# Optimization experiments

Hardware: AMD Instinct MI355X
Metric: run time of the kernel (lower is better)

Reference implementation:

```python
import jax, jax.numpy as jnp
import numpy as np

N_NODES = 100000
N_EDGES = 800000
VOCAB = 100
D_FEAT = 10
D = 64
EPS = 1e-8  # torch F.cosine_similarity eps


def setup_inputs() -> dict:
    key = jax.random.key(0)
    ks = jax.random.split(key, 8)
    return {
        "nodes": jax.random.randint(ks[0], (N_NODES,), 0, VOCAB),
        "edges": jax.random.randint(ks[1], (N_EDGES, 2), 0, N_NODES),
        "features": jax.random.normal(ks[2], (N_NODES, D_FEAT), dtype=jnp.float32),
        "node_emb": jax.random.normal(ks[3], (VOCAB, D), dtype=jnp.float32),
        "feat_W": jax.random.normal(ks[4], (D, D_FEAT), dtype=jnp.float32) * 0.1,
        "feat_b": jnp.zeros((D,), dtype=jnp.float32),
        "conv1_W": jax.random.normal(ks[5], (D, D), dtype=jnp.float32) * 0.1,
        "conv1_b": jnp.zeros((D,), dtype=jnp.float32),
        "pattern_emb": jax.random.normal(ks[6], (VOCAB, D), dtype=jnp.float32),
        "pattern_id": 42,  # hash(node_type) % 100
    }


def reference(nodes, edges, features, node_emb, feat_W, feat_b,
              conv1_W, conv1_b, pattern_emb, pattern_id):
    # initial embeddings: type embedding + linear feature projection  [N, D]
    embeds = node_emb[nodes] + (features @ feat_W.T + feat_b)

    src, dst = edges[:, 0], edges[:, 1]
    for _ in range(2):  # fixed 2 message-passing rounds (structural loop)
        # scatter-add messages from src to dst (order-independent sum)
        agg = jnp.zeros_like(embeds).at[dst].add(embeds[src])
        embeds = jax.nn.relu((embeds + agg) @ conv1_W.T + conv1_b)

    # cosine similarity of each node embedding against the pattern embedding
    p = pattern_emb[pattern_id]  # [D]
    num = embeds @ p  # [N]
    denom = jnp.maximum(jnp.linalg.norm(embeds, axis=1), EPS) * \
            jnp.maximum(jnp.linalg.norm(p), EPS)
    return num / denom  # [N] match scores
```

## Files before the change

kernel.cpp:

```cpp
#include <hip/hip_runtime.h>
#include <hip/hip_bf16.h>

#define N_NODES 100000
#define N_EDGES 800000
#define D 64
#define SCAN_B 256
#define NB1 ((N_NODES + SCAN_B - 1) / SCAN_B)
#define FILL_BLOCKS (N_EDGES / 256)
#define INIT_BLOCKS (N_NODES * D / 256)
#define CT 64
#define XS 68
#define OS 72

__device__ __forceinline__ unsigned short f2bf(float f) {
    union { float f; unsigned u; } v; v.f = f;
    unsigned r = v.u + 0x7fffu + ((v.u >> 16) & 1u);
    return (unsigned short)(r >> 16);
}
__device__ __forceinline__ float bf2f(unsigned short u) {
    return __uint_as_float(((unsigned)u) << 16);
}
__device__ __forceinline__ void acc_bf8(float acc[8], uint4 u) {
    acc[0] += __uint_as_float(u.x << 16);
    acc[1] += __uint_as_float(u.x & 0xffff0000u);
    acc[2] += __uint_as_float(u.y << 16);
    acc[3] += __uint_as_float(u.y & 0xffff0000u);
    acc[4] += __uint_as_float(u.z << 16);
    acc[5] += __uint_as_float(u.z & 0xffff0000u);
    acc[6] += __uint_as_float(u.w << 16);
    acc[7] += __uint_as_float(u.w & 0xffff0000u);
}

__global__ __launch_bounds__(256) void hist_rank_kernel(
        const int2* __restrict__ edges,
        int* __restrict__ deg,
        int* __restrict__ rank) {
    int t = blockIdx.x * 256 + threadIdx.x;
    int2 e = edges[t];
    rank[t] = atomicAdd(&deg[e.y], 1);
}

__global__ void scan1_kernel(const int* __restrict__ deg,
                             int* __restrict__ row_ptr,
                             int* __restrict__ bsum) {
    __shared__ int tmp[SCAN_B];
    int t = threadIdx.x;
    int i = blockIdx.x * SCAN_B + t;
    int v = (i < N_NODES) ? deg[i] : 0;
    tmp[t] = v;
    __syncthreads();
#pragma unroll
    for (int off = 1; off < SCAN_B; off <<= 1) {
        int a = (t >= off) ? tmp[t - off] : 0;
        __syncthreads();
        tmp[t] += a;
        __syncthreads();
    }
    if (i < N_NODES) row_ptr[i] = tmp[t] - v;
    if (t == SCAN_B - 1) bsum[blockIdx.x] = tmp[t];
}

__global__ void scan23_kernel(int* __restrict__ row_ptr,
                              const int* __restrict__ bsum) {
    __shared__ int red[SCAN_B];
    int t = threadIdx.x;
    int partial = 0;
    if (t < blockIdx.x && t < NB1) partial += bsum[t];
    int t2 = t + 256;
    if (t2 < blockIdx.x && t2 < NB1) partial += bsum[t2];
    red[t] = partial;
    __syncthreads();
#pragma unroll
    for (int off = 128; off > 0; off >>= 1) {
        if (t < off) red[t] += red[t + off];
        __syncthreads();
    }
    int boff = red[0];
    int i = blockIdx.x * SCAN_B + t;
    if (i < N_NODES) row_ptr[i] += boff;
    if (i == 0) row_ptr[N_NODES] = N_EDGES;
}

__global__ __launch_bounds__(256) void fill_init_kernel(
        const int2* __restrict__ edges,
        const int* __restrict__ rank,
        const int* __restrict__ rowp,
        int* __restrict__ col,
        const int* __restrict__ nodes,
        const float* __restrict__ features,
        const float* __restrict__ node_emb,
        const float* __restrict__ feat_W,
        const float* __restrict__ feat_b,
        unsigned short* __restrict__ embeds) {
    if (blockIdx.x < FILL_BLOCKS) {
        int t = blockIdx.x * 256 + threadIdx.x;
        int2 e = edges[t];
        col[rowp[e.y] + rank[t]] = e.x;
    } else {
        int tid = (blockIdx.x - FILL_BLOCKS) * 256 + threadIdx.x;
        int node = tid >> 6;
        int d = tid & 63;
        float acc = feat_b[d];
        const float* f = features + (size_t)node * 10;
        const float* w = feat_W + (size_t)d * 10;
#pragma unroll
        for (int j = 0; j < 10; ++j) acc += f[j] * w[j];
        embeds[tid] = f2bf(node_emb[(size_t)nodes[node] * D + d] + acc);
    }
}

template <bool SCORE>
__global__ __launch_bounds__(512, 8) void gconv_kernel(
        const unsigned short* __restrict__ emb_in,
        const int* __restrict__ rowp,
        const int* __restrict__ col,
        const float* __restrict__ W,
        const float* __restrict__ b,
        const float* __restrict__ pattern_emb,
        const int* __restrict__ pattern_id,
        unsigned short* __restrict__ emb_out,
        float* __restrict__ score_out) {
    __shared__ float Xs[CT][XS];
    __shared__ union {
        float W4[CT][XS];
        unsigned short Os[CT][OS];
    } u;
    __shared__ float ps[D];

    int t = threadIdx.x;
    int base = blockIdx.x * CT;
    int lane = t & 63;
    int wv = t >> 6;

    {
        int c = t & 15;
        int r = t >> 4;
#pragma unroll
        for (int p = 0; p < 2; ++p) {
            int rr = r + 32 * p;
            *((float4*)&u.W4[rr][4 * c]) = ((const float4*)(W + (size_t)rr * D))[c];
        }
    }
    if (SCORE && t < D) ps[t] = pattern_emb[(size_t)pattern_id[0] * D + t];

    int g = lane >> 3;
    int c8 = lane & 7;
    int rp = 0;
    if (lane <= 8) {
        int nidx = base + wv * 8 + lane;
        rp = rowp[nidx <= N_NODES ? nidx : N_NODES];
    }

    for (int nn = 0; nn < 8; ++nn) {
        int rl = wv * 8 + nn;
        int node = base + rl;
        int start = __shfl(rp, nn, 64);
        int end   = __shfl(rp, nn + 1, 64);

        float acc[8];
#pragma unroll
        for (int j = 0; j < 8; ++j) acc[j] = 0.f;
        if (g == 0 && node < N_NODES) {
            uint4 uu = ((const uint4*)(emb_in + (size_t)node * D))[c8];
            acc_bf8(acc, uu);
        }

        for (int b2 = start; b2 < end; b2 += 32) {
            int nb = end - b2; if (nb > 32) nb = 32;
            int idx = (lane < nb) ? col[b2 + lane] : 0;
#pragma unroll
            for (int r = 0; r < 4; ++r) {
                int s = r * 8 + g;
                int src = __shfl(idx, s, 64);
                if (s < nb) {
                    uint4 uu = ((const uint4*)(emb_in + (size_t)src * D))[c8];
                    acc_bf8(acc, uu);
                }
            }
        }

#pragma unroll
        for (int m = 8; m <= 32; m <<= 1)
#pragma unroll
            for (int j = 0; j < 8; ++j) acc[j] += __shfl_xor(acc[j], m, 64);

        if (g == 0) {
            *((float4*)&Xs[rl][8 * c8])     = make_float4(acc[0], acc[1], acc[2], acc[3]);
            *((float4*)&Xs[rl][8 * c8 + 4]) = make_float4(acc[4], acc[5], acc[6], acc[7]);
        }
    }
    __syncthreads();

    int i = t & 15;
    int j = t >> 4;
    float bj0 = b[j], bj1 = b[j + 32];

    float acc2[4][2] = {};
    for (int k4 = 0; k4 < 16; ++k4) {
        float4 xr[4], wr[2];
#pragma unroll
        for (int di = 0; di < 4; ++di) xr[di] = *((const float4*)&Xs[i + 16 * di][4 * k4]);
        wr[0] = *((const float4*)&u.W4[j][4 * k4]);
        wr[1] = *((const float4*)&u.W4[j + 32][4 * k4]);
#pragma unroll
        for (int di = 0; di < 4; ++di)
#pragma unroll
            for (int dj = 0; dj < 2; ++dj)
                acc2[di][dj] += xr[di].x * wr[dj].x + xr[di].y * wr[dj].y
                              + xr[di].z * wr[dj].z + xr[di].w * wr[dj].w;
    }

    if (!SCORE) {
        __syncthreads();
#pragma unroll
        for (int di = 0; di < 4; ++di) {
            u.Os[i + 16 * di][j]      = f2bf(fmaxf(acc2[di][0] + bj0, 0.f));
            u.Os[i + 16 * di][j + 32] = f2bf(fmaxf(acc2[di][1] + bj1, 0.f));
        }
        __syncthreads();
        int r = t >> 3, seg = t & 7;
        int node = base + r;
        if (node < N_NODES)
            ((uint4*)(emb_out + (size_t)node * D))[seg] = *((const uint4*)&u.Os[r][8 * seg]);
    } else {
        __syncthreads();
#pragma unroll
        for (int di = 0; di < 4; ++di) {
            Xs[i + 16 * di][j]      = fmaxf(acc2[di][0] + bj0, 0.f);
            Xs[i + 16 * di][j + 32] = fmaxf(acc2[di][1] + bj1, 0.f);
        }
        __syncthreads();
        if (t < CT) {
            float dot = 0.f, n2 = 0.f, pn = 0.f;
#pragma unroll 8
            for (int k = 0; k < D; ++k) {
                float yk = Xs[t][k];
                float pk = ps[k];
                dot += yk * pk; n2 += yk * yk; pn += pk * pk;
            }
            int node = base + t;
            if (node < N_NODES)
                score_out[node] = dot / (fmaxf(sqrtf(n2), 1e-8f) * fmaxf(sqrtf(pn), 1e-8f));
        }
    }
}

__global__ void init_embeds_kernel(const int* __restrict__ nodes,
                                   const float* __restrict__ features,
                                   const float* __restrict__ node_emb,
                                   const float* __restrict__ feat_W,
                                   const float* __restrict__ feat_b,
                                   float* __restrict__ embeds) {
    int tid = blockIdx.x * blockDim.x + threadIdx.x;
    if (tid >= N_NODES * D) return;
    int node = tid >> 6;
    int d = tid & 63;
    float acc = feat_b[d];
    const float* f = features + (size_t)node * 10;
    const float* w = feat_W + (size_t)d * 10;
#pragma unroll
    for (int j = 0; j < 10; ++j) acc += f[j] * w[j];
    embeds[tid] = node_emb[(size_t)nodes[node] * D + d] + acc;
}

__global__ void scatter_add_kernel(const int* __restrict__ edges,
                                   const float* __restrict__ embeds,
                                   float* __restrict__ agg) {
    int tid = blockIdx.x * blockDim.x + threadIdx.x;
    int edge = tid >> 6;
    int lane = tid & 63;
    if (edge >= N_EDGES) return;
    int src = edges[2 * edge + 0];
    int dst = edges[2 * edge + 1];
    atomicAdd(&agg[(size_t)dst * D + lane], embeds[(size_t)src * D + lane]);
}

__global__ void conv_inplace_kernel(const float* __restrict__ agg,
                                    const float* __restrict__ W,
                                    const float* __restrict__ b,
                                    float* __restrict__ embeds) {
    __shared__ float Ws[D * 65];
    __shared__ float xs[4][D];
    for (int i = threadIdx.x; i < D * D; i += blockDim.x) {
        int d = i >> 6, k = i & 63;
        Ws[d * 65 + k] = W[i];
    }
    __syncthreads();
    int lane_d = threadIdx.x & 63;
    int local_n = threadIdx.x >> 6;
    float bias = b[lane_d];
    const int n_chunks = (N_NODES + 3) / 4;
    for (int chunk = blockIdx.x; chunk < n_chunks; chunk += gridDim.x) {
        int node = chunk * 4 + local_n;
        if (node < N_NODES) {
            size_t base = (size_t)node * D + lane_d;
            xs[local_n][lane_d] = embeds[base] + agg[base];
        }
        __syncthreads();
        if (node < N_NODES) {
            float acc = bias;
#pragma unroll
            for (int k = 0; k < D; ++k) acc += xs[local_n][k] * Ws[lane_d * 65 + k];
            embeds[(size_t)node * D + lane_d] = fmaxf(acc, 0.0f);
        }
        __syncthreads();
    }
}

__global__ void final_score_kernel(const float* __restrict__ embeds,
                                   const float* __restrict__ pattern_emb,
                                   const int* __restrict__ pattern_id,
                                   float* __restrict__ out) {
    int lane = threadIdx.x & 63;
    int wave = threadIdx.x >> 6;
    int node = blockIdx.x * 4 + wave;
    int pid = pattern_id[0];
    float p = pattern_emb[(size_t)pid * D + lane];
    float pn = p * p;
#pragma unroll
    for (int m = 32; m > 0; m >>= 1) pn += __shfl_xor(pn, m, 64);
    if (node < N_NODES) {
        float e = embeds[(size_t)node * D + lane];
        float dot = e * p;
        float n2 = e * e;
#pragma unroll
        for (int m = 32; m > 0; m >>= 1) {
            dot += __shfl_xor(dot, m, 64);
            n2  += __shfl_xor(n2, m, 64);
        }
        if (lane == 0) {
            float denom = fmaxf(sqrtf(n2), 1e-8f) * fmaxf(sqrtf(pn), 1e-8f);
            out[node] = dot / denom;
        }
    }
}

extern "C" void kernel_launch(void* const* d_in, const int* in_sizes, int n_in,
                              void* d_out, int out_size, void* d_ws, size_t ws_size,
                              hipStream_t stream) {
    const int*   nodes       = (const int*)d_in[0];
    const int*   edges       = (const int*)d_in[1];
    const float* features    = (const float*)d_in[2];
    const float* node_emb    = (const float*)d_in[3];
    const float* feat_W      = (const float*)d_in[4];
    const float* feat_b      = (const float*)d_in[5];
    const float* conv1_W     = (const float*)d_in[6];
    const float* conv1_b     = (const float*)d_in[7];
    const float* pattern_emb = (const float*)d_in[8];
    const int*   pattern_id  = (const int*)d_in[9];
    float* out = (float*)d_out;

    const size_t emb_f32_bytes = (size_t)N_NODES * D * sizeof(float);
    const size_t emb_bf_bytes  = (size_t)N_NODES * D * 2;
    auto align256 = [](size_t x) { return (x + 255) & ~(size_t)255; };

    size_t o_embA = 0;
    size_t o_embB = o_embA + align256(emb_bf_bytes);
    size_t o_col  = o_embB + align256(emb_bf_bytes);
    size_t o_rank = o_col  + align256((size_t)N_EDGES * 4);
    size_t o_row  = o_rank + align256((size_t)N_EDGES * 4);
    size_t o_deg  = o_row  + align256((size_t)(N_NODES + 1) * 4);
    size_t o_bsum = o_deg  + align256((size_t)N_NODES * 4);
    size_t need   = o_bsum + align256((size_t)NB1 * 4);

    char* ws = (char*)d_ws;

    if (ws_size >= need) {
        unsigned short* embA = (unsigned short*)(ws + o_embA);
        unsigned short* embB = (unsigned short*)(ws + o_embB);
        int*   col  = (int*)(ws + o_col);
        int*   rank = (int*)(ws + o_rank);
        int*   rowp = (int*)(ws + o_row);
        int*   deg  = (int*)(ws + o_deg);
        int*   bsum = (int*)(ws + o_bsum);

        hipMemsetAsync(deg, 0, (size_t)N_NODES * 4, stream);
        hist_rank_kernel<<<FILL_BLOCKS, 256, 0, stream>>>((const int2*)edges, deg, rank);
        scan1_kernel<<<NB1, SCAN_B, 0, stream>>>(deg, rowp, bsum);
        scan23_kernel<<<NB1, SCAN_B, 0, stream>>>(rowp, bsum);
        fill_init_kernel<<<FILL_BLOCKS + INIT_BLOCKS, 256, 0, stream>>>(
            (const int2*)edges, rank, rowp, col,
            nodes, features, node_emb, feat_W, feat_b, embA);

        const int conv_grid = (N_NODES + CT - 1) / CT;

        gconv_kernel<false><<<conv_grid, 512, 0, stream>>>(
            embA, rowp, col, conv1_W, conv1_b, pattern_emb, pattern_id, embB, nullptr);
        gconv_kernel<true><<<conv_grid, 512, 0, stream>>>(
            embB, rowp, col, conv1_W, conv1_b, pattern_emb, pattern_id, nullptr, out);
    } else {
        float* embeds = (float*)ws;
        float* agg = (float*)(ws + align256(emb_f32_bytes));
        init_embeds_kernel<<<(N_NODES * D + 255) / 256, 256, 0, stream>>>(
            nodes, features, node_emb, feat_W, feat_b, embeds);
        for (int it = 0; it < 2; ++it) {
            hipMemsetAsync(agg, 0, emb_f32_bytes, stream);
            long long total = (long long)N_EDGES * 64;
            scatter_add_kernel<<<(int)((total + 255) / 256), 256, 0, stream>>>(edges, embeds, agg);
            conv_inplace_kernel<<<2048, 256, 0, stream>>>(agg, conv1_W, conv1_b, embeds);
        }
        final_score_kernel<<<(N_NODES + 3) / 4, 256, 0, stream>>>(
            embeds, pattern_emb, pattern_id, out);
    }
}
```

Measured before the change: 278.0 us.

## Restructure graph conv to one node per wavefront with in-register matvec

The conv kernel now assigns one node per 64-lane wavefront (4 nodes per 256-thread block) instead of 64 nodes per 512-thread block. The dense 64x64 transform is done per node in registers from a swizzled shared-memory copy of W, with a shuffle reduction, instead of a block-wide tiled GEMM. This removes the block-level syncs and the staging tiles in the epilogue, and the cosine score is computed with wave shuffles. In exchange every block reloads the full 16KB W into shared memory for only four nodes, and there are more shuffles per node.

Measured after the change: 332.4 us. 1.2x slower.

```diff
diff --git a/kernel.cpp b/kernel.cpp
--- a/kernel.cpp
+++ b/kernel.cpp
@@ -8,9 +8,6 @@
 #define NB1 ((N_NODES + SCAN_B - 1) / SCAN_B)
 #define FILL_BLOCKS (N_EDGES / 256)
 #define INIT_BLOCKS (N_NODES * D / 256)
-#define CT 64
-#define XS 68
-#define OS 72
 
 __device__ __forceinline__ unsigned short f2bf(float f) {
     union { float f; unsigned u; } v; v.f = f;
@@ -29,6 +26,9 @@
     acc[5] += __uint_as_float(u.z & 0xffff0000u);
     acc[6] += __uint_as_float(u.w << 16);
     acc[7] += __uint_as_float(u.w & 0xffff0000u);
+}
+__device__ __forceinline__ unsigned pack2bf(float a, float b) {
+    return (unsigned)f2bf(a) | ((unsigned)f2bf(b) << 16);
 }
 
 __global__ __launch_bounds__(256) void hist_rank_kernel(
@@ -110,7 +110,7 @@
 }
 
 template <bool SCORE>
-__global__ __launch_bounds__(512, 8) void gconv_kernel(
+__global__ __launch_bounds__(256, 6) void gatherconv_kernel(
         const unsigned short* __restrict__ emb_in,
         const int* __restrict__ rowp,
         const int* __restrict__ col,
@@ -120,128 +120,103 @@
         const int* __restrict__ pattern_id,
         unsigned short* __restrict__ emb_out,
         float* __restrict__ score_out) {
-    __shared__ float Xs[CT][XS];
-    __shared__ union {
-        float W4[CT][XS];
-        unsigned short Os[CT][OS];
-    } u;
-    __shared__ float ps[D];
+    __shared__ float Wl[4096];
+    __shared__ float bl[64];
+    __shared__ float ps[64];
 
     int t = threadIdx.x;
-    int base = blockIdx.x * CT;
+
+#pragma unroll
+    for (int q = 0; q < 4; ++q) {
+        int v = t + 256 * q;
+        float4 w4 = ((const float4*)W)[v];
+        int d  = v >> 4;
+        int k4 = v & 15;
+        int c  = k4 >> 1;
+        int i0 = (k4 & 1) * 4;
+        int slot = ((d & 7) * 64) + ((d >> 3) * 8) + c;
+        *((float4*)&Wl[slot * 8 + i0]) = w4;
+    }
+    if (t < 64) bl[t] = b[t];
+    if (SCORE && t < 64) ps[t] = pattern_emb[(size_t)pattern_id[0] * D + t];
+    __syncthreads();
+
     int lane = t & 63;
-    int wv = t >> 6;
-
-    {
-        int c = t & 15;
-        int r = t >> 4;
-#pragma unroll
-        for (int p = 0; p < 2; ++p) {
-            int rr = r + 32 * p;
-            *((float4*)&u.W4[rr][4 * c]) = ((const float4*)(W + (size_t)rr * D))[c];
-        }
-    }
-    if (SCORE && t < D) ps[t] = pattern_emb[(size_t)pattern_id[0] * D + t];
-
+    int wv   = t >> 6;
+    int node = blockIdx.x * 4 + wv;
     int g = lane >> 3;
-    int c8 = lane & 7;
-    int rp = 0;
-    if (lane <= 8) {
-        int nidx = base + wv * 8 + lane;
-        rp = rowp[nidx <= N_NODES ? nidx : N_NODES];
-    }
-
-    for (int nn = 0; nn < 8; ++nn) {
-        int rl = wv * 8 + nn;
-        int node = base + rl;
-        int start = __shfl(rp, nn, 64);
-        int end   = __shfl(rp, nn + 1, 64);
-
-        float acc[8];
-#pragma unroll
-        for (int j = 0; j < 8; ++j) acc[j] = 0.f;
-        if (g == 0 && node < N_NODES) {
-            uint4 uu = ((const uint4*)(emb_in + (size_t)node * D))[c8];
-            acc_bf8(acc, uu);
-        }
-
-        for (int b2 = start; b2 < end; b2 += 32) {
-            int nb = end - b2; if (nb > 32) nb = 32;
-            int idx = (lane < nb) ? col[b2 + lane] : 0;
-#pragma unroll
-            for (int r = 0; r < 4; ++r) {
-                int s = r * 8 + g;
-                int src = __shfl(idx, s, 64);
-                if (s < nb) {
-                    uint4 uu = ((const uint4*)(emb_in + (size_t)src * D))[c8];
-                    acc_bf8(acc, uu);
-                }
+    int c = lane & 7;
+
+    int start = rowp[node];
+    int end   = rowp[node + 1];
+
+    float acc[8];
+#pragma unroll
+    for (int j = 0; j < 8; ++j) acc[j] = 0.f;
+    if (g == 0) {
+        uint4 u = ((const uint4*)(emb_in + (size_t)node * D))[c];
+        acc_bf8(acc, u);
+    }
+
+    for (int base = start; base < end; base += 32) {
+        int nb = end - base; if (nb > 32) nb = 32;
+        int idx = (lane < nb) ? col[base + lane] : 0;
+#pragma unroll
+        for (int r = 0; r < 4; ++r) {
+            int s = r * 8 + g;
+            int src = __shfl(idx, s, 64);
+            if (s < nb) {
+                uint4 u = ((const uint4*)(emb_in + (size_t)src * D))[c];
+                acc_bf8(acc, u);
             }
         }
-
-#pragma unroll
-        for (int m = 8; m <= 32; m <<= 1)
-#pragma unroll
-            for (int j = 0; j < 8; ++j) acc[j] += __shfl_xor(acc[j], m, 64);
-
-        if (g == 0) {
-            *((float4*)&Xs[rl][8 * c8])     = make_float4(acc[0], acc[1], acc[2], acc[3]);
-            *((float4*)&Xs[rl][8 * c8 + 4]) = make_float4(acc[4], acc[5], acc[6], acc[7]);
-        }
-    }
-    __syncthreads();
-
-    int i = t & 15;
-    int j = t >> 4;
-    float bj0 = b[j], bj1 = b[j + 32];
-
-    float acc2[4][2] = {};
-    for (int k4 = 0; k4 < 16; ++k4) {
-        float4 xr[4], wr[2];
-#pragma unroll
-        for (int di = 0; di < 4; ++di) xr[di] = *((const float4*)&Xs[i + 16 * di][4 * k4]);
-        wr[0] = *((const float4*)&u.W4[j][4 * k4]);
-        wr[1] = *((const float4*)&u.W4[j + 32][4 * k4]);
-#pragma unroll
-        for (int di = 0; di < 4; ++di)
-#pragma unroll
-            for (int dj = 0; dj < 2; ++dj)
-                acc2[di][dj] += xr[di].x * wr[dj].x + xr[di].y * wr[dj].y
-                              + xr[di].z * wr[dj].z + xr[di].w * wr[dj].w;
-    }
+    }
+#pragma unroll
+    for (int m = 8; m <= 32; m <<= 1) {
+#pragma unroll
+        for (int j = 0; j < 8; ++j) acc[j] += __shfl_xor(acc[j], m, 64);
+    }
+
+    float y[8];
+#pragma unroll
+    for (int j = 0; j < 8; ++j) {
+        const float4* wp = (const float4*)&Wl[(j * 64 + lane) * 8];
+        float4 w0 = wp[0], w1 = wp[1];
+        y[j] = acc[0] * w0.x + acc[1] * w0.y + acc[2] * w0.z + acc[3] * w0.w
+             + acc[4] * w1.x + acc[5] * w1.y + acc[6] * w1.z + acc[7] * w1.w;
+    }
+#pragma unroll
+    for (int m = 1; m <= 4; m <<= 1) {
+#pragma unroll
+        for (int j = 0; j < 8; ++j) y[j] += __shfl_xor(y[j], m, 64);
+    }
+#pragma unroll
+    for (int j = 0; j < 8; ++j) y[j] = fmaxf(y[j] + bl[g * 8 + j], 0.f);
 
     if (!SCORE) {
-        __syncthreads();
-#pragma unroll
-        for (int di = 0; di < 4; ++di) {
-            u.Os[i + 16 * di][j]      = f2bf(fmaxf(acc2[di][0] + bj0, 0.f));
-            u.Os[i + 16 * di][j + 32] = f2bf(fmaxf(acc2[di][1] + bj1, 0.f));
-        }
-        __syncthreads();
-        int r = t >> 3, seg = t & 7;
-        int node = base + r;
-        if (node < N_NODES)
-            ((uint4*)(emb_out + (size_t)node * D))[seg] = *((const uint4*)&u.Os[r][8 * seg]);
+        if (c == 0) {
+            uint4 p;
+            p.x = pack2bf(y[0], y[1]);
+            p.y = pack2bf(y[2], y[3]);
+            p.z = pack2bf(y[4], y[5]);
+            p.w = pack2bf(y[6], y[7]);
+            ((uint4*)(emb_out + (size_t)node * D))[g] = p;
+        }
     } else {
-        __syncthreads();
-#pragma unroll
-        for (int di = 0; di < 4; ++di) {
-            Xs[i + 16 * di][j]      = fmaxf(acc2[di][0] + bj0, 0.f);
-            Xs[i + 16 * di][j + 32] = fmaxf(acc2[di][1] + bj1, 0.f);
-        }
-        __syncthreads();
-        if (t < CT) {
-            float dot = 0.f, n2 = 0.f, pn = 0.f;
-#pragma unroll 8
-            for (int k = 0; k < D; ++k) {
-                float yk = Xs[t][k];
-                float pk = ps[k];
-                dot += yk * pk; n2 += yk * yk; pn += pk * pk;
-            }
-            int node = base + t;
-            if (node < N_NODES)
-                score_out[node] = dot / (fmaxf(sqrtf(n2), 1e-8f) * fmaxf(sqrtf(pn), 1e-8f));
-        }
+        float dot = 0.f, n2 = 0.f, pn = 0.f;
+#pragma unroll
+        for (int j = 0; j < 8; ++j) {
+            float pk = ps[g * 8 + j];
+            dot += y[j] * pk; n2 += y[j] * y[j]; pn += pk * pk;
+        }
+#pragma unroll
+        for (int m = 8; m <= 32; m <<= 1) {
+            dot += __shfl_xor(dot, m, 64);
+            n2  += __shfl_xor(n2,  m, 64);
+            pn  += __shfl_xor(pn,  m, 64);
+        }
+        if (lane == 0)
+            score_out[node] = dot / (fmaxf(sqrtf(n2), 1e-8f) * fmaxf(sqrtf(pn), 1e-8f));
     }
 }
 
@@ -382,11 +357,9 @@
             (const int2*)edges, rank, rowp, col,
             nodes, features, node_emb, feat_W, feat_b, embA);
 
-        const int conv_grid = (N_NODES + CT - 1) / CT;
-
-        gconv_kernel<false><<<conv_grid, 512, 0, stream>>>(
+        gatherconv_kernel<false><<<N_NODES / 4, 256, 0, stream>>>(
             embA, rowp, col, conv1_W, conv1_b, pattern_emb, pattern_id, embB, nullptr);
-        gconv_kernel<true><<<conv_grid, 512, 0, stream>>>(
+        gatherconv_kernel<true><<<N_NODES / 4, 256, 0, stream>>>(
             embB, rowp, col, conv1_W, conv1_b, pattern_emb, pattern_id, nullptr, out);
     } else {
         float* embeds = (float*)ws;
```
